# Kernel optimization log

Hardware: AMD Instinct MI355X
Metric: run time of the kernel (lower is better)

## Reference

```python
import jax, jax.numpy as jnp
import numpy as np

B, S, D = 16, 2048, 768  # batch, padded subword length, roberta hidden dim


def setup_inputs() -> dict:
    key = jax.random.key(0)
    k1, k2 = jax.random.split(key)
    robert_embed = jax.random.normal(k1, (B, S, D), dtype=jnp.float32)
    # Non-decreasing per-row segment ids: contiguous runs of equal ids are the
    # subword spans that merge_list would average; singleton runs pass through.
    seg_ids = jnp.sort(jax.random.randint(k2, (B, S), 0, S, dtype=jnp.int32), axis=-1)
    return {"robert_embed": robert_embed, "seg_ids": seg_ids}


def reference(robert_embed, seg_ids):
    # Segment-mean gather/scatter: out[b, w] = mean_{p: seg_ids[b,p]==w} x[b, p]
    b, s, d = robert_embed.shape
    w = s  # output word slots (<= s); empty slots yield zeros
    flat_seg = (seg_ids + (w * jnp.arange(b, dtype=seg_ids.dtype))[:, None]).reshape(-1)
    x_flat = robert_embed.reshape(-1, d)
    sums = jax.ops.segment_sum(x_flat, flat_seg, num_segments=b * w)  # [b*w, d]
    counts = jax.ops.segment_sum(
        jnp.ones((b * s,), dtype=robert_embed.dtype), flat_seg, num_segments=b * w
    )
    out = sums / jnp.maximum(counts, 1)[:, None]
    return out.reshape(b, w, d)
```

## Files before the change

### kernel.cpp

```cpp
#include <hip/hip_runtime.h>

#define BB 16
#define SS 2048
#define DD 768
#define D4 192
#define P  16
#define CPR (SS / P)
#define PF 8
#define NT 192

typedef float vfloat4 __attribute__((ext_vector_type(4)));

__global__ __launch_bounds__(NT) void seg_mean_stream(
    const float* __restrict__ x,
    const int*   __restrict__ seg,
    float*       __restrict__ out)
{
    __shared__ __align__(16) int sseg[SS];

    const int b     = blockIdx.x >> 7;
    const int chunk = blockIdx.x & (CPR - 1);
    const int p0 = chunk * P;
    const int p1 = p0 + P;
    const int t  = threadIdx.x;

    {
        const int4* s4 = (const int4*)(seg + (b << 11));
        int4* l4 = (int4*)sseg;
        #pragma unroll
        for (int i = 0; i < 3; ++i) {
            int idx = t + i * NT;
            if (idx < SS / 4) l4[idx] = s4[idx];
        }
    }
    __syncthreads();

    const int prev = (p0 == 0) ? -1 : sseg[p0 - 1];
    int p = p0;
    while (p < p1 && sseg[p] == prev) ++p;
    if (p >= p1) return;

    int pe = p1;
    while (pe < SS && sseg[pe] == sseg[pe - 1]) ++pe;

    const vfloat4* xrow = (const vfloat4*)(x + (((size_t)b) << 11) * DD);
    float* outrow = out + (((size_t)b) << 11) * DD;
    const vfloat4 z = (vfloat4){0.f, 0.f, 0.f, 0.f};

    int runid = sseg[p];
    for (int w = prev + 1; w < runid; ++w)
        __builtin_nontemporal_store(z, (vfloat4*)(outrow + (size_t)w * DD) + t);

    #define LDX(r) (xrow[(size_t)((r) < pe ? (r) : (pe - 1)) * D4 + t])
    vfloat4 v0 = LDX(p + 0), v1 = LDX(p + 1), v2 = LDX(p + 2), v3 = LDX(p + 3);
    vfloat4 v4 = LDX(p + 4), v5 = LDX(p + 5), v6 = LDX(p + 6), v7 = LDX(p + 7);

    vfloat4 sum = z;
    int cnt = 0;
    bool done = false;

    #define STEP(BUF) {                                                       \
        vfloat4 cur = BUF;                                                    \
        BUF = LDX(p + PF);                        \
        sum += cur; ++cnt;                                                    \
        int pn = p + 1;                                                       \
        int sn = (pn < SS) ? sseg[pn] : -2;                                   \
        if (sn != runid) {                                 \
            vfloat4 m = sum * (1.0f / (float)cnt);                            \
            __builtin_nontemporal_store(m,                                    \
                (vfloat4*)(outrow + (size_t)runid * DD) + t);                 \
            if (pn >= SS) {                      \
                for (int w = runid + 1; w < SS; ++w)                          \
                    __builtin_nontemporal_store(z,                            \
                        (vfloat4*)(outrow + (size_t)w * DD) + t);             \
                done = true;                                                  \
            } else if (pn >= p1) {                     \
                done = true;                                                  \
            } else {                                \
                for (int w = runid + 1; w < sn; ++w)                          \
                    __builtin_nontemporal_store(z,                            \
                        (vfloat4*)(outrow + (size_t)w * DD) + t);             \
                runid = sn; sum = z; cnt = 0;                                 \
            }                                                                 \
        }                                                                     \
        p = pn;                                                               \
    }

    while (!done) {
        STEP(v0); if (done) break;
        STEP(v1); if (done) break;
        STEP(v2); if (done) break;
        STEP(v3); if (done) break;
        STEP(v4); if (done) break;
        STEP(v5); if (done) break;
        STEP(v6); if (done) break;
        STEP(v7); if (done) break;
    }
    #undef STEP
    #undef LDX
}

extern "C" void kernel_launch(void* const* d_in, const int* in_sizes, int n_in,
                              void* d_out, int out_size, void* d_ws, size_t ws_size,
                              hipStream_t stream) {
    const float* x   = (const float*)d_in[0];
    const int*   seg = (const int*)d_in[1];
    float* out = (float*)d_out;

    int nBlocks = BB * CPR;
    seg_mean_stream<<<nBlocks, NT, 0, stream>>>(x, seg, out);
}
```

Before: 184.8 us.

## Use per-chunk prefix sums in LDS with eager bulk loads for segment means

Each block now loads all 16 rows of its chunk up front, forms a running prefix sum per thread and stores it in LDS, so each run's sum inside the chunk is one subtraction of two prefix entries. Only a 65-entry window of segment ids is staged instead of the full 2048-entry row, and the serial dependent load/add loop with prefetch is replaced by independent wide loads. Runs that spill past the chunk are finished by reading the extra rows straight from global memory. In exchange the kernel uses 48KB of LDS per block, which can reduce occupancy, and it reads every row of a chunk even when the block exits early because no run starts in it.

New measurement: 182.0 us. About the same (-1.5%).

```diff
diff --git a/kernel.cpp b/kernel.cpp
--- a/kernel.cpp
+++ b/kernel.cpp
@@ -6,98 +6,78 @@
 #define D4 192
 #define P  16
 #define CPR (SS / P)
-#define PF 8
 #define NT 192
+#define SEGW 64
 
 typedef float vfloat4 __attribute__((ext_vector_type(4)));
 
-__global__ __launch_bounds__(NT) void seg_mean_stream(
+__global__ __launch_bounds__(NT) void seg_mean_v6(
     const float* __restrict__ x,
     const int*   __restrict__ seg,
     float*       __restrict__ out)
 {
-    __shared__ __align__(16) int sseg[SS];
+    __shared__ __align__(16) vfloat4 q[P * D4];
+    __shared__ int sseg[SEGW + 1];
 
     const int b     = blockIdx.x >> 7;
     const int chunk = blockIdx.x & (CPR - 1);
-    const int p0 = chunk * P;
+    const int p0 = chunk << 4;
     const int p1 = p0 + P;
     const int t  = threadIdx.x;
+    const int* segrow = seg + (b << 11);
 
-    {
-        const int4* s4 = (const int4*)(seg + (b << 11));
-        int4* l4 = (int4*)sseg;
-        #pragma unroll
-        for (int i = 0; i < 3; ++i) {
-            int idx = t + i * NT;
-            if (idx < SS / 4) l4[idx] = s4[idx];
-        }
+    if (t <= SEGW) {
+        int idx = p0 - 1 + t;
+        int v;
+        if (idx < 0) v = -1;
+        else if (idx >= SS) v = -2;
+        else v = segrow[idx];
+        sseg[t] = v;
     }
+
+    const vfloat4* xrow = (const vfloat4*)(x + ((size_t)(b << 11) + p0) * DD);
+    vfloat4 v[P];
+    #pragma unroll
+    for (int r = 0; r < P; ++r) v[r] = xrow[(size_t)r * D4 + t];
+    #pragma unroll
+    for (int r = 1; r < P; ++r) v[r] += v[r - 1];
+    #pragma unroll
+    for (int r = 0; r < P; ++r) q[r * D4 + t] = v[r];
     __syncthreads();
 
-    const int prev = (p0 == 0) ? -1 : sseg[p0 - 1];
+    int prev = sseg[0];
+    #define SID(pp) (((pp) - p0 + 1 <= SEGW) ? sseg[(pp) - p0 + 1] : segrow[(pp)])
     int p = p0;
-    while (p < p1 && sseg[p] == prev) ++p;
+    while (p < p1 && SID(p) == prev) ++p;
     if (p >= p1) return;
 
-    int pe = p1;
-    while (pe < SS && sseg[pe] == sseg[pe - 1]) ++pe;
+    float* outrow = out + (size_t)(b << 11) * DD;
+    const vfloat4 z = {0.f, 0.f, 0.f, 0.f};
+    int w = prev + 1;
+    while (p < p1) {
+        int id = SID(p);
+        int e = p + 1;
+        while (e < SS && SID(e) == id) ++e;
 
-    const vfloat4* xrow = (const vfloat4*)(x + (((size_t)b) << 11) * DD);
-    float* outrow = out + (((size_t)b) << 11) * DD;
-    const vfloat4 z = (vfloat4){0.f, 0.f, 0.f, 0.f};
+        for (; w < id; ++w)
+            __builtin_nontemporal_store(z, (vfloat4*)(outrow + (size_t)w * DD) + t);
 
-    int runid = sseg[p];
-    for (int w = prev + 1; w < runid; ++w)
-        __builtin_nontemporal_store(z, (vfloat4*)(outrow + (size_t)w * DD) + t);
+        int eh = (e < p1 ? e : p1);
+        vfloat4 s = q[(eh - 1 - p0) * D4 + t];
+        if (p > p0) s -= q[(p - 1 - p0) * D4 + t];
+        for (int r = p1; r < e; ++r)
+            s += ((const vfloat4*)(x + ((size_t)(b << 11) + r) * DD))[t];
 
-    #define LDX(r) (xrow[(size_t)((r) < pe ? (r) : (pe - 1)) * D4 + t])
-    vfloat4 v0 = LDX(p + 0), v1 = LDX(p + 1), v2 = LDX(p + 2), v3 = LDX(p + 3);
-    vfloat4 v4 = LDX(p + 4), v5 = LDX(p + 5), v6 = LDX(p + 6), v7 = LDX(p + 7);
+        float inv = 1.0f / (float)(e - p);
+        __builtin_nontemporal_store(s * inv, (vfloat4*)(outrow + (size_t)id * DD) + t);
+        w = id + 1;
 
-    vfloat4 sum = z;
-    int cnt = 0;
-    bool done = false;
-
-    #define STEP(BUF) {                                                       \
-        vfloat4 cur = BUF;                                                    \
-        BUF = LDX(p + PF);                        \
-        sum += cur; ++cnt;                                                    \
-        int pn = p + 1;                                                       \
-        int sn = (pn < SS) ? sseg[pn] : -2;                                   \
-        if (sn != runid) {                                 \
-            vfloat4 m = sum * (1.0f / (float)cnt);                            \
-            __builtin_nontemporal_store(m,                                    \
-                (vfloat4*)(outrow + (size_t)runid * DD) + t);                 \
-            if (pn >= SS) {                      \
-                for (int w = runid + 1; w < SS; ++w)                          \
-                    __builtin_nontemporal_store(z,                            \
-                        (vfloat4*)(outrow + (size_t)w * DD) + t);             \
-                done = true;                                                  \
-            } else if (pn >= p1) {                     \
-                done = true;                                                  \
-            } else {                                \
-                for (int w = runid + 1; w < sn; ++w)                          \
-                    __builtin_nontemporal_store(z,                            \
-                        (vfloat4*)(outrow + (size_t)w * DD) + t);             \
-                runid = sn; sum = z; cnt = 0;                                 \
-            }                                                                 \
-        }                                                                     \
-        p = pn;                                                               \
+        if (e >= SS)
+            for (; w < SS; ++w)
+                __builtin_nontemporal_store(z, (vfloat4*)(outrow + (size_t)w * DD) + t);
+        p = e;
     }
-
-    while (!done) {
-        STEP(v0); if (done) break;
-        STEP(v1); if (done) break;
-        STEP(v2); if (done) break;
-        STEP(v3); if (done) break;
-        STEP(v4); if (done) break;
-        STEP(v5); if (done) break;
-        STEP(v6); if (done) break;
-        STEP(v7); if (done) break;
-    }
-    #undef STEP
-    #undef LDX
+    #undef SID
 }
 
 extern "C" void kernel_launch(void* const* d_in, const int* in_sizes, int n_in,
@@ -108,5 +88,5 @@
     float* out = (float*)d_out;
 
     int nBlocks = BB * CPR;
-    seg_mean_stream<<<nBlocks, NT, 0, stream>>>(x, seg, out);
+    seg_mean_v6<<<nBlocks, NT, 0, stream>>>(x, seg, out);
 }
```
